# Kernel optimization log

Measured on AMD Instinct MI355X. Metric: run time of the kernel, lower is better.

## Reference

```python
import jax, jax.numpy as jnp
import numpy as np


def setup_inputs() -> dict:
    key = jax.random.key(0)
    ks = jax.random.split(key, 8)
    B, N, D, S = 4, 16384, 512, 512
    x = jax.random.normal(ks[0], (B, N, D), dtype=jnp.float32)
    jx = jnp.sort(jax.random.randint(ks[1], (N,), 0, S, dtype=jnp.int64))
    scale = 1.0 / np.sqrt(D)
    Wf = jax.random.normal(ks[2], (D, D), dtype=jnp.float32) * scale
    bf = jax.random.normal(ks[3], (D,), dtype=jnp.float32) * scale
    Wg = jax.random.normal(ks[4], (D, D), dtype=jnp.float32) * scale
    bg = jax.random.normal(ks[5], (D,), dtype=jnp.float32) * scale
    Wh = jax.random.normal(ks[6], (D, D), dtype=jnp.float32) * scale
    bh = jax.random.normal(ks[7], (D,), dtype=jnp.float32) * scale
    return {"x": x, "jx": jx, "num_segments": S, "Wf": Wf, "bf": bf,
            "Wg": Wg, "bg": bg, "Wh": Wh, "bh": bh}


def reference(x, jx, num_segments, Wf, bf, Wg, bg, Wh, bh):
    # x: [B, N, D]; jx: [N] segment ids; segments along axis 1.
    fx = jnp.einsum('bnd,ed->bne', x, Wf) + bf  # f(x)
    gx = jnp.einsum('bnd,ed->bne', x, Wg) + bg  # g(x)
    # move N to leading axis so jax.ops.segment_* apply: [N, B, D]
    gx_t = jnp.transpose(gx, (1, 0, 2))
    fx_t = jnp.transpose(fx, (1, 0, 2))
    # scatter_softmax over segments (numerically stable)
    m = jax.ops.segment_max(gx_t, jx, num_segments=num_segments)  # [S, B, D]
    e = jnp.exp(gx_t - m[jx])
    denom = jax.ops.segment_sum(e, jx, num_segments=num_segments)  # [S, B, D]
    w = e / denom[jx]  # [N, B, D]
    # weighted scatter-sum
    y_t = jax.ops.segment_sum(fx_t * w, jx, num_segments=num_segments)  # [S, B, D]
    y = jnp.transpose(y_t, (1, 0, 2))  # [B, S, D]
    hy = jnp.einsum('bsd,ed->bse', y, Wh) + bh
    # expand=True: gather back to per-element
    return hy[:, jx]  # [B, N, D]
```

## Files before the change

### kernel.cpp

```cpp
#include <hip/hip_runtime.h>
#include <stdint.h>

#define B_ 4
#define N_ 16384
#define D_ 512
#define S_ 512

typedef __attribute__((ext_vector_type(8))) short bf16x8;
typedef __attribute__((ext_vector_type(4))) float f32x4;

__device__ __forceinline__ float bf2f(unsigned short u) {
  union { unsigned int i; float f; } v; v.i = ((unsigned int)u) << 16; return v.f;
}
__device__ __forceinline__ unsigned short f2bf(float f) {
  unsigned int x = __float_as_uint(f);
  return (unsigned short)((x + 0x7FFFu + ((x >> 16) & 1u)) >> 16);
}
__device__ __forceinline__ float ldf(const void* p, long i, bool f32) {
  return f32 ? ((const float*)p)[i] : bf2f(((const unsigned short*)p)[i]);
}
__device__ __forceinline__ void gl_lds16(void* lds_base, const void* g) {
  __builtin_amdgcn_global_load_lds(
      (const __attribute__((address_space(1))) unsigned int*)g,
      (__attribute__((address_space(3))) unsigned int*)lds_base,
      16, 0, 0);
}

__device__ __forceinline__ bool jx_is_i64(const int* jx32) { return jx32[N_ - 1] == 0; }
__device__ __forceinline__ int seg_id(const int* jx32, int n, bool i64) {
  return i64 ? jx32[2 * n] : jx32[n];
}

__device__ __forceinline__ bool classify_f32(const unsigned short* x, int* cnt) {
  int c = 0;
#pragma unroll
  for (int i = 0; i < 8; i++) {
    unsigned short w = x[threadIdx.x * 8 + i];
    int e = (w >> 7) & 0xFF;
    if (e == 0 || (e >= 100 && e <= 140)) c++;
  }
  cnt[threadIdx.x] = c;
  __syncthreads();
  for (int s = 128; s > 0; s >>= 1) {
    if ((int)threadIdx.x < s) cnt[threadIdx.x] += cnt[threadIdx.x + s];
    __syncthreads();
  }
  bool f32 = cnt[0] < 1843;
  __syncthreads();
  return f32;
}

__global__ __launch_bounds__(256)
void prep_all(const void* __restrict__ x, const int* __restrict__ jx,
              const void* __restrict__ Wf, const void* __restrict__ bfv,
              const void* __restrict__ Wg, const void* __restrict__ bgv,
              const void* __restrict__ Wh, const void* __restrict__ bhv,
              unsigned short* __restrict__ xb, unsigned short* __restrict__ Wfg,
              unsigned short* __restrict__ biasfg, unsigned short* __restrict__ Whb,
              unsigned short* __restrict__ bhb, int* __restrict__ segst,
              int* __restrict__ flag) {
  const int blk = blockIdx.x, tid = threadIdx.x;
  __shared__ int cnt[256];
  const bool f32 = classify_f32((const unsigned short*)x, cnt);
  if (blk >= 19462) {
    if (blk == 19462 && tid == 0) flag[0] = f32 ? 1 : 0;
    int s = (blk - 19462) * 256 + tid;
    if (s > S_) return;
    bool i64 = jx_is_i64(jx);
    int lo = 0, hi = N_;
    while (lo < hi) {
      int mid = (lo + hi) >> 1;
      if (seg_id(jx, mid, i64) < s) lo = mid + 1; else hi = mid;
    }
    segst[s] = lo;
    return;
  }
  if (blk < 16384) {
    const size_t i0 = ((size_t)blk * 256 + tid) * 8;
    bf16x8 v;
    if (f32) {
      const float4* p = (const float4*)((const float*)x + i0);
      float4 a = p[0], b = p[1];
      v[0]=f2bf(a.x); v[1]=f2bf(a.y); v[2]=f2bf(a.z); v[3]=f2bf(a.w);
      v[4]=f2bf(b.x); v[5]=f2bf(b.y); v[6]=f2bf(b.z); v[7]=f2bf(b.w);
    } else {
      v = *(const bf16x8*)((const unsigned short*)x + i0);
    }
    *(bf16x8*)(xb + i0) = v;
  } else {
    int idx = (blk - 16384) * 256 + tid;
    if (idx < 524288) {
      int e = idx >> 9, d = idx & 511;
      float v = (e < 512) ? ldf(Wf, (long)e * 512 + d, f32)
                          : ldf(Wg, (long)(e - 512) * 512 + d, f32);
      Wfg[idx] = f2bf(v);
    } else if (idx < 786432) {
      Whb[idx - 524288] = f2bf(ldf(Wh, idx - 524288, f32));
    } else if (idx < 787456) {
      int j = idx - 786432;
      biasfg[j] = f2bf(j < 512 ? ldf(bfv, j, f32) : ldf(bgv, j - 512, f32));
    } else if (idx < 787968) {
      bhb[idx - 787456] = f2bf(ldf(bhv, idx - 787456, f32));
    }
  }
}

#define BK 32

__global__ __launch_bounds__(256, 2)
void gemm_fg(const unsigned short* __restrict__ A, const unsigned short* __restrict__ Bm,
             const unsigned short* __restrict__ bias,
             unsigned short* __restrict__ Cf, unsigned short* __restrict__ Cg) {
  __shared__ __align__(16) unsigned short As[128 * BK];
  __shared__ __align__(16) unsigned short Bs[128 * BK];
  const int L = blockIdx.x;
  const int xcd = L & 7, local = L >> 3;
  const int tm = xcd * 64 + local / 8;
  const int tn = local % 8;
  const int m0 = tm * 128, n0 = tn * 128;

  const int tid  = threadIdx.x;
  const int w    = tid >> 6;
  const int lane = tid & 63;
  const int wm   = w >> 1, wn = w & 1;
  const int l15  = lane & 15, l4 = lane >> 4;
  const int srow = lane >> 2;
  const int scol = (lane & 3) * 8;

  f32x4 acc[4][4];
#pragma unroll
  for (int i = 0; i < 4; i++)
#pragma unroll
    for (int j = 0; j < 4; j++) acc[i][j] = (f32x4){0.f, 0.f, 0.f, 0.f};

  for (int kt = 0; kt < 512; kt += BK) {
    __syncthreads();
#pragma unroll
    for (int r = 0; r < 2; r++) {
      const int rb = (r * 4 + w) * 16;
      gl_lds16(&As[rb * BK], A + (size_t)(m0 + rb + srow) * 512 + kt + scol);
      gl_lds16(&Bs[rb * BK], Bm + (size_t)(n0 + rb + srow) * 512 + kt + scol);
    }
    __syncthreads();

    bf16x8 a[4], bb[4];
#pragma unroll
    for (int i = 0; i < 4; i++)
      a[i] = *(const bf16x8*)&As[(wm * 64 + i * 16 + l15) * BK + l4 * 8];
#pragma unroll
    for (int j = 0; j < 4; j++)
      bb[j] = *(const bf16x8*)&Bs[(wn * 64 + j * 16 + l15) * BK + l4 * 8];
#pragma unroll
    for (int i = 0; i < 4; i++)
#pragma unroll
      for (int j = 0; j < 4; j++)
        acc[i][j] = __builtin_amdgcn_mfma_f32_16x16x32_bf16(a[i], bb[j], acc[i][j], 0, 0, 0);
  }

#pragma unroll
  for (int j = 0; j < 4; j++) {
    const int col = n0 + wn * 64 + j * 16 + l15;
    const float bv = bf2f(bias[col]);
    unsigned short* base = (col < 512) ? Cf : Cg;
    const int cc = col & 511;
#pragma unroll
    for (int i = 0; i < 4; i++) {
      const int rowb = m0 + wm * 64 + i * 16 + l4 * 4;
#pragma unroll
      for (int r = 0; r < 4; r++)
        base[(size_t)(rowb + r) * 512 + cc] = f2bf(acc[i][j][r] + bv);
    }
  }
}

__global__ __launch_bounds__(256)
void seg_softmax(const unsigned short* __restrict__ f, const unsigned short* __restrict__ g,
                 const int* __restrict__ segst, unsigned short* __restrict__ y) {
  const int s = blockIdx.x * 2 + (threadIdx.x >> 7);
  const int b = blockIdx.y;
  const int d0 = (threadIdx.x & 127) * 4;
  const int st = segst[s], en = segst[s + 1];
  float den0=0.f, den1=0.f, den2=0.f, den3=0.f;
  float y0=0.f, y1=0.f, y2=0.f, y3=0.f;
  int n = st;
  for (; n + 1 < en; n += 2) {
    const size_t offA = (size_t)(b * N_ + n) * 512 + d0;
    const size_t offB = offA + 512;
    const uint2 fpA = *(const uint2*)(f + offA);
    const uint2 gpA = *(const uint2*)(g + offA);
    const uint2 fpB = *(const uint2*)(f + offB);
    const uint2 gpB = *(const uint2*)(g + offB);
    {
      const float f0 = bf2f((unsigned short)fpA.x), f1 = bf2f((unsigned short)(fpA.x >> 16));
      const float f2 = bf2f((unsigned short)fpA.y), f3 = bf2f((unsigned short)(fpA.y >> 16));
      const float g0 = bf2f((unsigned short)gpA.x), g1 = bf2f((unsigned short)(gpA.x >> 16));
      const float g2 = bf2f((unsigned short)gpA.y), g3 = bf2f((unsigned short)(gpA.y >> 16));
      const float e0 = __expf(g0), e1 = __expf(g1), e2 = __expf(g2), e3 = __expf(g3);
      den0 += e0; den1 += e1; den2 += e2; den3 += e3;
      y0 += f0 * e0; y1 += f1 * e1; y2 += f2 * e2; y3 += f3 * e3;
    }
    {
      const float f0 = bf2f((unsigned short)fpB.x), f1 = bf2f((unsigned short)(fpB.x >> 16));
      const float f2 = bf2f((unsigned short)fpB.y), f3 = bf2f((unsigned short)(fpB.y >> 16));
      const float g0 = bf2f((unsigned short)gpB.x), g1 = bf2f((unsigned short)(gpB.x >> 16));
      const float g2 = bf2f((unsigned short)gpB.y), g3 = bf2f((unsigned short)(gpB.y >> 16));
      const float e0 = __expf(g0), e1 = __expf(g1), e2 = __expf(g2), e3 = __expf(g3);
      den0 += e0; den1 += e1; den2 += e2; den3 += e3;
      y0 += f0 * e0; y1 += f1 * e1; y2 += f2 * e2; y3 += f3 * e3;
    }
  }
  if (n < en) {
    const size_t off = (size_t)(b * N_ + n) * 512 + d0;
    const uint2 fp = *(const uint2*)(f + off);
    const uint2 gp = *(const uint2*)(g + off);
    const float f0 = bf2f((unsigned short)fp.x), f1 = bf2f((unsigned short)(fp.x >> 16));
    const float f2 = bf2f((unsigned short)fp.y), f3 = bf2f((unsigned short)(fp.y >> 16));
    const float g0 = bf2f((unsigned short)gp.x), g1 = bf2f((unsigned short)(gp.x >> 16));
    const float g2 = bf2f((unsigned short)gp.y), g3 = bf2f((unsigned short)(gp.y >> 16));
    const float e0 = __expf(g0), e1 = __expf(g1), e2 = __expf(g2), e3 = __expf(g3);
    den0 += e0; den1 += e1; den2 += e2; den3 += e3;
    y0 += f0 * e0; y1 += f1 * e1; y2 += f2 * e2; y3 += f3 * e3;
  }
  uint2 o;
  if (en > st) {
    o.x = (unsigned int)f2bf(y0 / den0) | ((unsigned int)f2bf(y1 / den1) << 16);
    o.y = (unsigned int)f2bf(y2 / den2) | ((unsigned int)f2bf(y3 / den3) << 16);
  } else { o.x = 0u; o.y = 0u; }
  *(uint2*)(y + (size_t)(b * S_ + s) * 512 + d0) = o;
}

__global__ __launch_bounds__(256)
void gemm_hy(const unsigned short* __restrict__ y, const unsigned short* __restrict__ Whb,
             const unsigned short* __restrict__ bhb, unsigned short* __restrict__ hy) {
  __shared__ __align__(16) unsigned short As[64 * 32];
  __shared__ __align__(16) unsigned short Bs[64 * 32];
  const int tid = threadIdx.x;
  const int w = tid >> 6, lane = tid & 63;
  const int l15 = lane & 15, l4 = lane >> 4;
  const int m0 = (blockIdx.x >> 3) * 64, c0 = (blockIdx.x & 7) * 64;
  const int srow = lane >> 2, scol = (lane & 3) * 8;

  f32x4 acc[4];
#pragma unroll
  for (int j = 0; j < 4; j++) acc[j] = (f32x4){0.f, 0.f, 0.f, 0.f};

  for (int kt = 0; kt < 512; kt += 32) {
    __syncthreads();
    gl_lds16(&As[(w * 16) * 32], y   + (size_t)(m0 + w * 16 + srow) * 512 + kt + scol);
    gl_lds16(&Bs[(w * 16) * 32], Whb + (size_t)(c0 + w * 16 + srow) * 512 + kt + scol);
    __syncthreads();
    bf16x8 a = *(const bf16x8*)&As[(w * 16 + l15) * 32 + l4 * 8];
#pragma unroll
    for (int j = 0; j < 4; j++) {
      bf16x8 bb = *(const bf16x8*)&Bs[(j * 16 + l15) * 32 + l4 * 8];
      acc[j] = __builtin_amdgcn_mfma_f32_16x16x32_bf16(a, bb, acc[j], 0, 0, 0);
    }
  }
#pragma unroll
  for (int j = 0; j < 4; j++) {
    const float bv = bf2f(bhb[c0 + j * 16 + l15]);
#pragma unroll
    for (int r = 0; r < 4; r++)
      hy[(size_t)(m0 + w * 16 + l4 * 4 + r) * 512 + c0 + j * 16 + l15] =
          f2bf(acc[j][r] + bv);
  }
}

__global__ __launch_bounds__(256)
void gather_out(const unsigned short* __restrict__ hy, const int* __restrict__ jx,
                void* __restrict__ out, const int* __restrict__ flag) {
  const bool f32 = flag[0] != 0;
  const int gid  = blockIdx.x * 256 + threadIdx.x;
  const int wid  = gid >> 6;
  const int lane = gid & 63;
  const int b = wid >> 14;
  const int n = wid & (N_ - 1);
  const bool i64 = jx_is_i64(jx);
  const int s = seg_id(jx, n, i64);
  const bf16x8 v = *(const bf16x8*)(hy + (size_t)(b * S_ + s) * 512 + lane * 8);
  if (f32) {
    float* dst = (float*)out + (size_t)wid * 512 + lane * 8;
    float4 lo, hi;
    lo.x=bf2f((unsigned short)v[0]); lo.y=bf2f((unsigned short)v[1]);
    lo.z=bf2f((unsigned short)v[2]); lo.w=bf2f((unsigned short)v[3]);
    hi.x=bf2f((unsigned short)v[4]); hi.y=bf2f((unsigned short)v[5]);
    hi.z=bf2f((unsigned short)v[6]); hi.w=bf2f((unsigned short)v[7]);
    *(float4*)dst = lo;
    *(float4*)(dst + 4) = hi;
  } else {
    *(bf16x8*)((unsigned short*)out + (size_t)wid * 512 + lane * 8) = v;
  }
}

extern "C" void kernel_launch(void* const* d_in, const int* in_sizes, int n_in,
                              void* d_out, int out_size, void* d_ws, size_t ws_size,
                              hipStream_t stream) {
  const void* x  = d_in[0];
  const int* jx  = (const int*)d_in[1];
  const void* Wf = d_in[3];
  const void* bf = d_in[4];
  const void* Wg = d_in[5];
  const void* bg = d_in[6];
  const void* Wh = d_in[7];
  const void* bh = d_in[8];

  char* ws = (char*)d_ws;
  int* flag              = (int*)(ws + 0);
  int* segst             = (int*)(ws + 4096);
  unsigned short* biasfg = (unsigned short*)(ws + 8192);
  unsigned short* bhb    = (unsigned short*)(ws + 16384);
  unsigned short* Wfg    = (unsigned short*)(ws + 32768);
  unsigned short* Whb    = (unsigned short*)(ws + 1081344);
  unsigned short* y_ws   = (unsigned short*)(ws + 1605632);
  unsigned short* hy_ws  = (unsigned short*)(ws + 3702784);
  unsigned short* xb     = (unsigned short*)(ws + 8388608);
  unsigned short* fbuf   = (unsigned short*)d_out;
  unsigned short* gbuf   = (unsigned short*)d_out + (size_t)B_ * N_ * D_;

  prep_all<<<19465, 256, 0, stream>>>(x, jx, Wf, bf, Wg, bg, Wh, bh,
                                      xb, Wfg, biasfg, Whb, bhb, segst, flag);
  gemm_fg<<<4096, 256, 0, stream>>>(xb, Wfg, biasfg, fbuf, gbuf);
  seg_softmax<<<dim3(256, B_), 256, 0, stream>>>(fbuf, gbuf, segst, y_ws);
  gemm_hy<<<256, 256, 0, stream>>>(y_ws, Whb, bhb, hy_ws);
  gather_out<<<16384, 256, 0, stream>>>(hy_ws, jx, d_out, flag);
}
```

Measured before the change: 395.1 us.

## Rewrite fused f/g GEMM as 256x256 tile with double-buffered swizzled LDS pipeline

```diff
diff --git a/kernel.cpp b/kernel.cpp
--- a/kernel.cpp
+++ b/kernel.cpp
@@ -105,70 +105,139 @@
   }
 }
 
-#define BK 32
-
-__global__ __launch_bounds__(256, 2)
+#define NKT 8
+
+#define RD_A(QM)                                                              \
+  _Pragma("unroll")                                                           \
+  for (int rf = 0; rf < 4; ++rf) {                                            \
+    const int arow = wm * 128 + (QM) * 64 + rf * 16 + l15;                    \
+    af[rf][0] = *(const bf16x8*)((const char*)Ac + arow * 128 + s0);          \
+    af[rf][1] = *(const bf16x8*)((const char*)Ac + arow * 128 + (s0 ^ 64));   \
+  }
+
+#define RD_B(QN)                                                              \
+  _Pragma("unroll")                                                           \
+  for (int cf = 0; cf < 2; ++cf) {                                            \
+    const int brow = wn * 64 + (QN) * 32 + cf * 16 + l15;                     \
+    bq[cf][0] = *(const bf16x8*)((const char*)Bc + brow * 128 + s0);          \
+    bq[cf][1] = *(const bf16x8*)((const char*)Bc + brow * 128 + (s0 ^ 64));   \
+  }
+
+#define BAR_LG()                                                              \
+  __builtin_amdgcn_s_barrier();                                               \
+  asm volatile("s_waitcnt lgkmcnt(0)" ::: "memory");                          \
+  __builtin_amdgcn_sched_barrier(0);
+
+#define MFMA_Q(QM, QN)                                                        \
+  __builtin_amdgcn_s_setprio(1);                                              \
+  _Pragma("unroll")                                                           \
+  for (int rf = 0; rf < 4; ++rf) {                                            \
+    _Pragma("unroll")                                                         \
+    for (int cf = 0; cf < 2; ++cf) {                                          \
+      acc[(QM) * 4 + rf][(QN) * 2 + cf] =                                     \
+          __builtin_amdgcn_mfma_f32_16x16x32_bf16(                            \
+              af[rf][0], bq[cf][0], acc[(QM) * 4 + rf][(QN) * 2 + cf], 0, 0, 0); \
+      acc[(QM) * 4 + rf][(QN) * 2 + cf] =                                     \
+          __builtin_amdgcn_mfma_f32_16x16x32_bf16(                            \
+              af[rf][1], bq[cf][1], acc[(QM) * 4 + rf][(QN) * 2 + cf], 0, 0, 0); \
+    }                                                                         \
+  }                                                                           \
+  __builtin_amdgcn_s_setprio(0);
+
+#define STG(LB, GP, GBASE, RB, KT)                                            \
+  gl_lds16(&(LB)[((RB) + w8) * 64],                                           \
+           (GP) + (size_t)((GBASE) + (RB) + w8 + lr) * 512 +                  \
+               (size_t)(KT) * 64 + lsw)
+
+__global__ __launch_bounds__(512, 2)
 void gemm_fg(const unsigned short* __restrict__ A, const unsigned short* __restrict__ Bm,
              const unsigned short* __restrict__ bias,
              unsigned short* __restrict__ Cf, unsigned short* __restrict__ Cg) {
-  __shared__ __align__(16) unsigned short As[128 * BK];
-  __shared__ __align__(16) unsigned short Bs[128 * BK];
+  __shared__ __align__(16) unsigned short Al[2][256 * 64];
+  __shared__ __align__(16) unsigned short Bl[2][256 * 64];
+
   const int L = blockIdx.x;
   const int xcd = L & 7, local = L >> 3;
-  const int tm = xcd * 64 + local / 8;
-  const int tn = local % 8;
-  const int m0 = tm * 128, n0 = tn * 128;
+  const int tm = xcd * 32 + (local >> 2);
+  const int tn = local & 3;
+  const int m0 = tm * 256, n0 = tn * 256;
 
   const int tid  = threadIdx.x;
   const int w    = tid >> 6;
   const int lane = tid & 63;
-  const int wm   = w >> 1, wn = w & 1;
+  const int wm   = w >> 2, wn = w & 3;
   const int l15  = lane & 15, l4 = lane >> 4;
-  const int srow = lane >> 2;
-  const int scol = (lane & 3) * 8;
-
-  f32x4 acc[4][4];
-#pragma unroll
-  for (int i = 0; i < 4; i++)
+  const int w8  = w * 8;
+  const int lr  = lane >> 3;
+  const int lsw = ((lane & 7) ^ (lr & 7)) * 8;
+  const int s0  = ((l4 ^ (l15 & 7)) * 16);
+
+  f32x4 acc[8][4];
+#pragma unroll
+  for (int i = 0; i < 8; i++)
 #pragma unroll
     for (int j = 0; j < 4; j++) acc[i][j] = (f32x4){0.f, 0.f, 0.f, 0.f};
-
-  for (int kt = 0; kt < 512; kt += BK) {
-    __syncthreads();
-#pragma unroll
-    for (int r = 0; r < 2; r++) {
-      const int rb = (r * 4 + w) * 16;
-      gl_lds16(&As[rb * BK], A + (size_t)(m0 + rb + srow) * 512 + kt + scol);
-      gl_lds16(&Bs[rb * BK], Bm + (size_t)(n0 + rb + srow) * 512 + kt + scol);
-    }
-    __syncthreads();
-
-    bf16x8 a[4], bb[4];
-#pragma unroll
-    for (int i = 0; i < 4; i++)
-      a[i] = *(const bf16x8*)&As[(wm * 64 + i * 16 + l15) * BK + l4 * 8];
-#pragma unroll
-    for (int j = 0; j < 4; j++)
-      bb[j] = *(const bf16x8*)&Bs[(wn * 64 + j * 16 + l15) * BK + l4 * 8];
-#pragma unroll
-    for (int i = 0; i < 4; i++)
-#pragma unroll
-      for (int j = 0; j < 4; j++)
-        acc[i][j] = __builtin_amdgcn_mfma_f32_16x16x32_bf16(a[i], bb[j], acc[i][j], 0, 0, 0);
-  }
-
-#pragma unroll
-  for (int j = 0; j < 4; j++) {
-    const int col = n0 + wn * 64 + j * 16 + l15;
+  bf16x8 af[4][2];
+  bf16x8 bq[2][2];
+
+  STG(Al[0], A, m0, 0, 0);   STG(Al[0], A, m0, 128, 0);
+  STG(Al[0], A, m0, 64, 0);  STG(Al[0], A, m0, 192, 0);
+  STG(Bl[0], Bm, n0, 0, 0);  STG(Bl[0], Bm, n0, 64, 0);
+  STG(Bl[0], Bm, n0, 128, 0); STG(Bl[0], Bm, n0, 192, 0);
+  STG(Al[1], A, m0, 0, 1);   STG(Al[1], A, m0, 128, 1);
+  STG(Al[1], A, m0, 64, 1);  STG(Al[1], A, m0, 192, 1);
+  asm volatile("s_waitcnt vmcnt(4)" ::: "memory");
+  __builtin_amdgcn_s_barrier();
+
+#pragma unroll 2
+  for (int t = 0; t < NKT; ++t) {
+    const int c = t & 1;
+    const unsigned short* Ac = Al[c];
+    const unsigned short* Bc = Bl[c];
+    unsigned short* An = Al[c];
+    unsigned short* Bn = Bl[c ^ 1];
+    const bool stB = (t + 1 < NKT);
+    const bool stA = (t + 2 < NKT);
+
+    RD_A(0); RD_B(0);
+    if (stB) { STG(Bn, Bm, n0, 128, t + 1); STG(Bn, Bm, n0, 192, t + 1); }
+    BAR_LG();
+    MFMA_Q(0, 0);
+    __builtin_amdgcn_s_barrier();
+
+    RD_B(1);
+    if (stA) { STG(An, A, m0, 0, t + 2); STG(An, A, m0, 128, t + 2); }
+    BAR_LG();
+    MFMA_Q(0, 1);
+    __builtin_amdgcn_s_barrier();
+
+    RD_A(1); RD_B(0);
+    if (stB) { STG(Bn, Bm, n0, 0, t + 1); STG(Bn, Bm, n0, 64, t + 1); }
+    BAR_LG();
+    MFMA_Q(1, 0);
+    __builtin_amdgcn_s_barrier();
+
+    RD_B(1);
+    if (stA) { STG(An, A, m0, 64, t + 2); STG(An, A, m0, 192, t + 2); }
+    if (t >= NKT - 2) { asm volatile("s_waitcnt vmcnt(0)" ::: "memory"); }
+    else              { asm volatile("s_waitcnt vmcnt(2)" ::: "memory"); }
+    BAR_LG();
+    MFMA_Q(1, 1);
+    __builtin_amdgcn_s_barrier();
+  }
+
+#pragma unroll
+  for (int C = 0; C < 4; ++C) {
+    const int col = n0 + wn * 64 + C * 16 + l15;
     const float bv = bf2f(bias[col]);
     unsigned short* base = (col < 512) ? Cf : Cg;
     const int cc = col & 511;
 #pragma unroll
-    for (int i = 0; i < 4; i++) {
-      const int rowb = m0 + wm * 64 + i * 16 + l4 * 4;
-#pragma unroll
-      for (int r = 0; r < 4; r++)
-        base[(size_t)(rowb + r) * 512 + cc] = f2bf(acc[i][j][r] + bv);
+    for (int R = 0; R < 8; ++R) {
+      const int rowb = m0 + wm * 128 + R * 16 + l4 * 4;
+#pragma unroll
+      for (int r = 0; r < 4; ++r)
+        base[(size_t)(rowb + r) * 512 + cc] = f2bf(acc[R][C][r] + bv);
     }
   }
 }
@@ -319,7 +388,7 @@
 
   prep_all<<<19465, 256, 0, stream>>>(x, jx, Wf, bf, Wg, bg, Wh, bh,
                                       xb, Wfg, biasfg, Whb, bhb, segst, flag);
-  gemm_fg<<<4096, 256, 0, stream>>>(xb, Wfg, biasfg, fbuf, gbuf);
+  gemm_fg<<<1024, 512, 0, stream>>>(xb, Wfg, biasfg, fbuf, gbuf);
   seg_softmax<<<dim3(256, B_), 256, 0, stream>>>(fbuf, gbuf, segst, y_ws);
   gemm_hy<<<256, 256, 0, stream>>>(y_ws, Whb, bhb, hy_ws);
   gather_out<<<16384, 256, 0, stream>>>(hy_ws, jx, d_out, flag);
```

Measured after the change: 429.0 us. +8.6%, slower.

## Fuse segment softmax reduction into f/g GEMM epilogue with LDS atomics

Applied to the files above, without the earlier changes.

```diff
diff --git a/kernel.cpp b/kernel.cpp
--- a/kernel.cpp
+++ b/kernel.cpp
@@ -5,6 +5,7 @@
 #define N_ 16384
 #define D_ 512
 #define S_ 512
+#define NSL 32
 
 typedef __attribute__((ext_vector_type(8))) short bf16x8;
 typedef __attribute__((ext_vector_type(4))) float f32x4;
@@ -58,8 +59,12 @@
               unsigned short* __restrict__ xb, unsigned short* __restrict__ Wfg,
               unsigned short* __restrict__ biasfg, unsigned short* __restrict__ Whb,
               unsigned short* __restrict__ bhb, int* __restrict__ segst,
-              int* __restrict__ flag) {
+              int* __restrict__ flag, float4* __restrict__ zbuf) {
   const int blk = blockIdx.x, tid = threadIdx.x;
+  if (blk >= 19465) {
+    zbuf[(blk - 19465) * 256 + tid] = (float4){0.f, 0.f, 0.f, 0.f};
+    return;
+  }
   __shared__ int cnt[256];
   const bool f32 = classify_f32((const unsigned short*)x, cnt);
   if (blk >= 19462) {
@@ -105,19 +110,20 @@
   }
 }
 
-#define BK 32
-
 __global__ __launch_bounds__(256, 2)
-void gemm_fg(const unsigned short* __restrict__ A, const unsigned short* __restrict__ Bm,
-             const unsigned short* __restrict__ bias,
-             unsigned short* __restrict__ Cf, unsigned short* __restrict__ Cg) {
-  __shared__ __align__(16) unsigned short As[128 * BK];
-  __shared__ __align__(16) unsigned short Bs[128 * BK];
+void gemm_fg2(const unsigned short* __restrict__ A, const unsigned short* __restrict__ Wfg,
+              const unsigned short* __restrict__ biasfg, const int* __restrict__ jx,
+              float* __restrict__ gden, float* __restrict__ gnum) {
+  __shared__ __align__(16) unsigned short As[128 * 32];
+  __shared__ __align__(16) unsigned short Bs[256 * 32];
+  __shared__ float sden[NSL][128];
+  __shared__ float snum[NSL][128];
+
   const int L = blockIdx.x;
   const int xcd = L & 7, local = L >> 3;
-  const int tm = xcd * 64 + local / 8;
-  const int tn = local % 8;
-  const int m0 = tm * 128, n0 = tn * 128;
+  const int tm = xcd * 64 + (local >> 2);
+  const int td = local & 3;
+  const int m0 = tm * 128, d0 = td * 128;
 
   const int tid  = threadIdx.x;
   const int w    = tid >> 6;
@@ -125,108 +131,120 @@
   const int wm   = w >> 1, wn = w & 1;
   const int l15  = lane & 15, l4 = lane >> 4;
   const int srow = lane >> 2;
-  const int scol = (lane & 3) * 8;
-
-  f32x4 acc[4][4];
+  const int swz_s = (((lane & 3) ^ ((lane >> 2) & 3)) << 3);
+  const int swz_r = ((l4 ^ (l15 & 3)) << 3);
+
+#pragma unroll
+  for (int k = 0; k < NSL * 128 / 256; k++) {
+    const int idx = k * 256 + tid;
+    sden[idx >> 7][idx & 127] = 0.f;
+    snum[idx >> 7][idx & 127] = 0.f;
+  }
+
+  f32x4 acc[4][8];
 #pragma unroll
   for (int i = 0; i < 4; i++)
 #pragma unroll
-    for (int j = 0; j < 4; j++) acc[i][j] = (f32x4){0.f, 0.f, 0.f, 0.f};
-
-  for (int kt = 0; kt < 512; kt += BK) {
+    for (int j = 0; j < 8; j++) acc[i][j] = (f32x4){0.f, 0.f, 0.f, 0.f};
+
+  for (int kt = 0; kt < 512; kt += 32) {
     __syncthreads();
 #pragma unroll
     for (int r = 0; r < 2; r++) {
       const int rb = (r * 4 + w) * 16;
-      gl_lds16(&As[rb * BK], A + (size_t)(m0 + rb + srow) * 512 + kt + scol);
-      gl_lds16(&Bs[rb * BK], Bm + (size_t)(n0 + rb + srow) * 512 + kt + scol);
-    }
-    __syncthreads();
-
-    bf16x8 a[4], bb[4];
+      gl_lds16(&As[rb * 32], A + (size_t)(m0 + rb + srow) * 512 + kt + swz_s);
+    }
+#pragma unroll
+    for (int r = 0; r < 4; r++) {
+      const int rb = (r * 4 + w) * 16;
+      const int erow = d0 + (rb & 127) + ((rb >> 7) * 512);
+      gl_lds16(&Bs[rb * 32], Wfg + (size_t)(erow + srow) * 512 + kt + swz_s);
+    }
+    __syncthreads();
+
+    bf16x8 a[4];
 #pragma unroll
     for (int i = 0; i < 4; i++)
-      a[i] = *(const bf16x8*)&As[(wm * 64 + i * 16 + l15) * BK + l4 * 8];
-#pragma unroll
-    for (int j = 0; j < 4; j++)
-      bb[j] = *(const bf16x8*)&Bs[(wn * 64 + j * 16 + l15) * BK + l4 * 8];
-#pragma unroll
-    for (int i = 0; i < 4; i++)
+      a[i] = *(const bf16x8*)&As[(wm * 64 + i * 16 + l15) * 32 + swz_r];
+    {
+      bf16x8 bb[4];
 #pragma unroll
       for (int j = 0; j < 4; j++)
-        acc[i][j] = __builtin_amdgcn_mfma_f32_16x16x32_bf16(a[i], bb[j], acc[i][j], 0, 0, 0);
-  }
-
+        bb[j] = *(const bf16x8*)&Bs[(wn * 64 + j * 16 + l15) * 32 + swz_r];
+#pragma unroll
+      for (int i = 0; i < 4; i++)
+#pragma unroll
+        for (int j = 0; j < 4; j++)
+          acc[i][j] = __builtin_amdgcn_mfma_f32_16x16x32_bf16(a[i], bb[j], acc[i][j], 0, 0, 0);
+    }
+    {
+      bf16x8 bb[4];
+#pragma unroll
+      for (int j = 0; j < 4; j++)
+        bb[j] = *(const bf16x8*)&Bs[(128 + wn * 64 + j * 16 + l15) * 32 + swz_r];
+#pragma unroll
+      for (int i = 0; i < 4; i++)
+#pragma unroll
+        for (int j = 0; j < 4; j++)
+          acc[i][4 + j] = __builtin_amdgcn_mfma_f32_16x16x32_bf16(a[i], bb[j], acc[i][4 + j], 0, 0, 0);
+    }
+  }
+
+  const bool i64 = jx_is_i64(jx);
+  const int b = m0 >> 14;
+  const int nrow0 = m0 & (N_ - 1);
+  const int segbase = seg_id(jx, nrow0, i64);
+  float biasF[4], biasG[4];
 #pragma unroll
   for (int j = 0; j < 4; j++) {
-    const int col = n0 + wn * 64 + j * 16 + l15;
-    const float bv = bf2f(bias[col]);
-    unsigned short* base = (col < 512) ? Cf : Cg;
-    const int cc = col & 511;
-#pragma unroll
-    for (int i = 0; i < 4; i++) {
-      const int rowb = m0 + wm * 64 + i * 16 + l4 * 4;
-#pragma unroll
-      for (int r = 0; r < 4; r++)
-        base[(size_t)(rowb + r) * 512 + cc] = f2bf(acc[i][j][r] + bv);
+    const int d = d0 + wn * 64 + j * 16 + l15;
+    biasF[j] = bf2f(biasfg[d]);
+    biasG[j] = bf2f(biasfg[512 + d]);
+  }
+#pragma unroll
+  for (int i = 0; i < 4; i++) {
+#pragma unroll
+    for (int r = 0; r < 4; r++) {
+      const int n = nrow0 + wm * 64 + i * 16 + l4 * 4 + r;
+      const int sl = seg_id(jx, n, i64) - segbase;
+#pragma unroll
+      for (int j = 0; j < 4; j++) {
+        const float fv = acc[i][j][r] + biasF[j];
+        const float gv = acc[i][4 + j][r] + biasG[j];
+        const float e  = __expf(gv);
+        const float fe = fv * e;
+        const int dc = wn * 64 + j * 16 + l15;
+        if (sl < NSL) {
+          unsafeAtomicAdd(&sden[sl][dc], e);
+          unsafeAtomicAdd(&snum[sl][dc], fe);
+        } else {
+          const size_t off = ((size_t)b * S_ + segbase + sl) * 512 + d0 + dc;
+          unsafeAtomicAdd(&gden[off], e);
+          unsafeAtomicAdd(&gnum[off], fe);
+        }
+      }
+    }
+  }
+  __syncthreads();
+#pragma unroll
+  for (int k = 0; k < NSL * 128 / 256; k++) {
+    const int idx = k * 256 + tid;
+    const int sl = idx >> 7, dc = idx & 127;
+    const float dv = sden[sl][dc];
+    if (dv > 0.f) {
+      const size_t off = ((size_t)b * S_ + segbase + sl) * 512 + d0 + dc;
+      unsafeAtomicAdd(&gden[off], dv);
+      unsafeAtomicAdd(&gnum[off], snum[sl][dc]);
     }
   }
 }
 
 __global__ __launch_bounds__(256)
-void seg_softmax(const unsigned short* __restrict__ f, const unsigned short* __restrict__ g,
-                 const int* __restrict__ segst, unsigned short* __restrict__ y) {
-  const int s = blockIdx.x * 2 + (threadIdx.x >> 7);
-  const int b = blockIdx.y;
-  const int d0 = (threadIdx.x & 127) * 4;
-  const int st = segst[s], en = segst[s + 1];
-  float den0=0.f, den1=0.f, den2=0.f, den3=0.f;
-  float y0=0.f, y1=0.f, y2=0.f, y3=0.f;
-  int n = st;
-  for (; n + 1 < en; n += 2) {
-    const size_t offA = (size_t)(b * N_ + n) * 512 + d0;
-    const size_t offB = offA + 512;
-    const uint2 fpA = *(const uint2*)(f + offA);
-    const uint2 gpA = *(const uint2*)(g + offA);
-    const uint2 fpB = *(const uint2*)(f + offB);
-    const uint2 gpB = *(const uint2*)(g + offB);
-    {
-      const float f0 = bf2f((unsigned short)fpA.x), f1 = bf2f((unsigned short)(fpA.x >> 16));
-      const float f2 = bf2f((unsigned short)fpA.y), f3 = bf2f((unsigned short)(fpA.y >> 16));
-      const float g0 = bf2f((unsigned short)gpA.x), g1 = bf2f((unsigned short)(gpA.x >> 16));
-      const float g2 = bf2f((unsigned short)gpA.y), g3 = bf2f((unsigned short)(gpA.y >> 16));
-      const float e0 = __expf(g0), e1 = __expf(g1), e2 = __expf(g2), e3 = __expf(g3);
-      den0 += e0; den1 += e1; den2 += e2; den3 += e3;
-      y0 += f0 * e0; y1 += f1 * e1; y2 += f2 * e2; y3 += f3 * e3;
-    }
-    {
-      const float f0 = bf2f((unsigned short)fpB.x), f1 = bf2f((unsigned short)(fpB.x >> 16));
-      const float f2 = bf2f((unsigned short)fpB.y), f3 = bf2f((unsigned short)(fpB.y >> 16));
-      const float g0 = bf2f((unsigned short)gpB.x), g1 = bf2f((unsigned short)(gpB.x >> 16));
-      const float g2 = bf2f((unsigned short)gpB.y), g3 = bf2f((unsigned short)(gpB.y >> 16));
-      const float e0 = __expf(g0), e1 = __expf(g1), e2 = __expf(g2), e3 = __expf(g3);
-      den0 += e0; den1 += e1; den2 += e2; den3 += e3;
-      y0 += f0 * e0; y1 += f1 * e1; y2 += f2 * e2; y3 += f3 * e3;
-    }
-  }
-  if (n < en) {
-    const size_t off = (size_t)(b * N_ + n) * 512 + d0;
-    const uint2 fp = *(const uint2*)(f + off);
-    const uint2 gp = *(const uint2*)(g + off);
-    const float f0 = bf2f((unsigned short)fp.x), f1 = bf2f((unsigned short)(fp.x >> 16));
-    const float f2 = bf2f((unsigned short)fp.y), f3 = bf2f((unsigned short)(fp.y >> 16));
-    const float g0 = bf2f((unsigned short)gp.x), g1 = bf2f((unsigned short)(gp.x >> 16));
-    const float g2 = bf2f((unsigned short)gp.y), g3 = bf2f((unsigned short)(gp.y >> 16));
-    const float e0 = __expf(g0), e1 = __expf(g1), e2 = __expf(g2), e3 = __expf(g3);
-    den0 += e0; den1 += e1; den2 += e2; den3 += e3;
-    y0 += f0 * e0; y1 += f1 * e1; y2 += f2 * e2; y3 += f3 * e3;
-  }
-  uint2 o;
-  if (en > st) {
-    o.x = (unsigned int)f2bf(y0 / den0) | ((unsigned int)f2bf(y1 / den1) << 16);
-    o.y = (unsigned int)f2bf(y2 / den2) | ((unsigned int)f2bf(y3 / den3) << 16);
-  } else { o.x = 0u; o.y = 0u; }
-  *(uint2*)(y + (size_t)(b * S_ + s) * 512 + d0) = o;
+void norm_y(const float* __restrict__ gden, const float* __restrict__ gnum,
+            unsigned short* __restrict__ y) {
+  const int idx = blockIdx.x * 256 + threadIdx.x;
+  const float d = gden[idx];
+  y[idx] = (d > 0.f) ? f2bf(gnum[idx] / d) : (unsigned short)0;
 }
 
 __global__ __launch_bounds__(256)
@@ -314,13 +332,14 @@
   unsigned short* y_ws   = (unsigned short*)(ws + 1605632);
   unsigned short* hy_ws  = (unsigned short*)(ws + 3702784);
   unsigned short* xb     = (unsigned short*)(ws + 8388608);
-  unsigned short* fbuf   = (unsigned short*)d_out;
-  unsigned short* gbuf   = (unsigned short*)d_out + (size_t)B_ * N_ * D_;
-
-  prep_all<<<19465, 256, 0, stream>>>(x, jx, Wf, bf, Wg, bg, Wh, bh,
-                                      xb, Wfg, biasfg, Whb, bhb, segst, flag);
-  gemm_fg<<<4096, 256, 0, stream>>>(xb, Wfg, biasfg, fbuf, gbuf);
-  seg_softmax<<<dim3(256, B_), 256, 0, stream>>>(fbuf, gbuf, segst, y_ws);
+  float* gden = (float*)d_out;
+  float* gnum = (float*)d_out + 1048576;
+
+  prep_all<<<21513, 256, 0, stream>>>(x, jx, Wf, bf, Wg, bg, Wh, bh,
+                                      xb, Wfg, biasfg, Whb, bhb, segst, flag,
+                                      (float4*)d_out);
+  gemm_fg2<<<2048, 256, 0, stream>>>(xb, Wfg, biasfg, jx, gden, gnum);
+  norm_y<<<4096, 256, 0, stream>>>(gden, gnum, y_ws);
   gemm_hy<<<256, 256, 0, stream>>>(y_ws, Whb, bhb, hy_ws);
   gather_out<<<16384, 256, 0, stream>>>(hy_ws, jx, d_out, flag);
 }
```

Measured after the change: 677.3 us. +71.4%, slower.

## Hoist dtype classification into own kernel; double GEMM K-tile with XOR-swizzled LDS

Applied to the files above, without the earlier changes.

```diff
diff --git a/kernel.cpp b/kernel.cpp
--- a/kernel.cpp
+++ b/kernel.cpp
@@ -31,11 +31,14 @@
   return i64 ? jx32[2 * n] : jx32[n];
 }
 
-__device__ __forceinline__ bool classify_f32(const unsigned short* x, int* cnt) {
+__global__ __launch_bounds__(256)
+void classify_k(const void* __restrict__ x, int* __restrict__ flag) {
+  __shared__ int cnt[256];
   int c = 0;
+  const unsigned short* xs = (const unsigned short*)x;
 #pragma unroll
   for (int i = 0; i < 8; i++) {
-    unsigned short w = x[threadIdx.x * 8 + i];
+    unsigned short w = xs[threadIdx.x * 8 + i];
     int e = (w >> 7) & 0xFF;
     if (e == 0 || (e >= 100 && e <= 140)) c++;
   }
@@ -45,9 +48,7 @@
     if ((int)threadIdx.x < s) cnt[threadIdx.x] += cnt[threadIdx.x + s];
     __syncthreads();
   }
-  bool f32 = cnt[0] < 1843;
-  __syncthreads();
-  return f32;
+  if (threadIdx.x == 0) flag[0] = (cnt[0] < 1843) ? 1 : 0;
 }
 
 __global__ __launch_bounds__(256)
@@ -58,12 +59,9 @@
               unsigned short* __restrict__ xb, unsigned short* __restrict__ Wfg,
               unsigned short* __restrict__ biasfg, unsigned short* __restrict__ Whb,
               unsigned short* __restrict__ bhb, int* __restrict__ segst,
-              int* __restrict__ flag) {
+              const int* __restrict__ flag) {
   const int blk = blockIdx.x, tid = threadIdx.x;
-  __shared__ int cnt[256];
-  const bool f32 = classify_f32((const unsigned short*)x, cnt);
   if (blk >= 19462) {
-    if (blk == 19462 && tid == 0) flag[0] = f32 ? 1 : 0;
     int s = (blk - 19462) * 256 + tid;
     if (s > S_) return;
     bool i64 = jx_is_i64(jx);
@@ -75,6 +73,7 @@
     segst[s] = lo;
     return;
   }
+  const bool f32 = flag[0] != 0;
   if (blk < 16384) {
     const size_t i0 = ((size_t)blk * 256 + tid) * 8;
     bf16x8 v;
@@ -105,7 +104,7 @@
   }
 }
 
-#define BK 32
+#define BK 64
 
 __global__ __launch_bounds__(256, 2)
 void gemm_fg(const unsigned short* __restrict__ A, const unsigned short* __restrict__ Bm,
@@ -124,8 +123,9 @@
   const int lane = tid & 63;
   const int wm   = w >> 1, wn = w & 1;
   const int l15  = lane & 15, l4 = lane >> 4;
-  const int srow = lane >> 2;
-  const int scol = (lane & 3) * 8;
+  const int srow8 = lane >> 3;
+  const int ssw   = ((lane & 7) ^ (srow8 & 7)) * 8;
+  const int rsw   = l15 & 7;
 
   f32x4 acc[4][4];
 #pragma unroll
@@ -136,25 +136,35 @@
   for (int kt = 0; kt < 512; kt += BK) {
     __syncthreads();
 #pragma unroll
-    for (int r = 0; r < 2; r++) {
-      const int rb = (r * 4 + w) * 16;
-      gl_lds16(&As[rb * BK], A + (size_t)(m0 + rb + srow) * 512 + kt + scol);
-      gl_lds16(&Bs[rb * BK], Bm + (size_t)(n0 + rb + srow) * 512 + kt + scol);
-    }
-    __syncthreads();
-
-    bf16x8 a[4], bb[4];
+    for (int r = 0; r < 4; r++) {
+      const int rb = r * 32 + w * 8;
+      gl_lds16(&As[rb * BK], A  + (size_t)(m0 + rb + srow8) * 512 + kt + ssw);
+      gl_lds16(&Bs[rb * BK], Bm + (size_t)(n0 + rb + srow8) * 512 + kt + ssw);
+    }
+    __syncthreads();
+
+    bf16x8 a[4][2], bb[4][2];
+#pragma unroll
+    for (int i = 0; i < 4; i++) {
+      const int row = wm * 64 + i * 16 + l15;
+#pragma unroll
+      for (int kk = 0; kk < 2; kk++)
+        a[i][kk] = *(const bf16x8*)&As[row * BK + (((l4 + kk * 4) ^ rsw) << 3)];
+    }
+#pragma unroll
+    for (int j = 0; j < 4; j++) {
+      const int row = wn * 64 + j * 16 + l15;
+#pragma unroll
+      for (int kk = 0; kk < 2; kk++)
+        bb[j][kk] = *(const bf16x8*)&Bs[row * BK + (((l4 + kk * 4) ^ rsw) << 3)];
+    }
 #pragma unroll
     for (int i = 0; i < 4; i++)
-      a[i] = *(const bf16x8*)&As[(wm * 64 + i * 16 + l15) * BK + l4 * 8];
-#pragma unroll
-    for (int j = 0; j < 4; j++)
-      bb[j] = *(const bf16x8*)&Bs[(wn * 64 + j * 16 + l15) * BK + l4 * 8];
-#pragma unroll
-    for (int i = 0; i < 4; i++)
-#pragma unroll
-      for (int j = 0; j < 4; j++)
-        acc[i][j] = __builtin_amdgcn_mfma_f32_16x16x32_bf16(a[i], bb[j], acc[i][j], 0, 0, 0);
+#pragma unroll
+      for (int j = 0; j < 4; j++) {
+        acc[i][j] = __builtin_amdgcn_mfma_f32_16x16x32_bf16(a[i][0], bb[j][0], acc[i][j], 0, 0, 0);
+        acc[i][j] = __builtin_amdgcn_mfma_f32_16x16x32_bf16(a[i][1], bb[j][1], acc[i][j], 0, 0, 0);
+      }
   }
 
 #pragma unroll
@@ -317,6 +327,7 @@
   unsigned short* fbuf   = (unsigned short*)d_out;
   unsigned short* gbuf   = (unsigned short*)d_out + (size_t)B_ * N_ * D_;
 
+  classify_k<<<1, 256, 0, stream>>>(x, flag);
   prep_all<<<19465, 256, 0, stream>>>(x, jx, Wf, bf, Wg, bg, Wh, bh,
                                       xb, Wfg, biasfg, Whb, bhb, segst, flag);
   gemm_fg<<<4096, 256, 0, stream>>>(xb, Wfg, biasfg, fbuf, gbuf);
```

Result: faster. 370.0 us (-6.4%).
